# Kernel optimization log

Measured on AMD Instinct MI355X. Metric: run time of the kernel, lower is better.

Reference implementation:

```python
import jax, jax.numpy as jnp
import numpy as np

D_MODEL = 1024
D_FF = 4096
N_HEADS = 16
D_HEAD = D_MODEL // N_HEADS
BSZ, SEQ = 2, 2048
EPS = 1e-6


def layer_norm(x, lam, beta):
    # torch impl: (x - mu) / (std_biased + eps) * lambda + beta
    mu = jnp.mean(x, axis=-1, keepdims=True)
    sigma = jnp.sqrt(jnp.mean((x - mu) ** 2, axis=-1, keepdims=True)) + EPS
    return (x - mu) / sigma * lam + beta


def setup_inputs() -> dict:
    key = jax.random.key(0)
    ks = jax.random.split(key, 10)
    s = 0.02
    x = jax.random.normal(ks[0], (BSZ, SEQ, D_MODEL), dtype=jnp.float32)
    mask = jnp.ones((BSZ, 1, 1, SEQ), dtype=jnp.int32)
    # nn.Linear weights stored [out, in]; y = x @ W.T
    Wq = jax.random.normal(ks[1], (D_MODEL, D_MODEL), dtype=jnp.float32) * s
    Wk = jax.random.normal(ks[2], (D_MODEL, D_MODEL), dtype=jnp.float32) * s
    Wv = jax.random.normal(ks[3], (D_MODEL, D_MODEL), dtype=jnp.float32) * s
    Wo = jax.random.normal(ks[4], (D_MODEL, D_MODEL), dtype=jnp.float32) * s
    w1 = jax.random.normal(ks[5], (D_FF, D_MODEL), dtype=jnp.float32) * s
    b1 = jnp.zeros((D_FF,), dtype=jnp.float32)
    w2 = jax.random.normal(ks[6], (D_MODEL, D_FF), dtype=jnp.float32) * s
    b2 = jnp.zeros((D_MODEL,), dtype=jnp.float32)
    g1 = jnp.ones((D_MODEL,), dtype=jnp.float32)
    be1 = jnp.zeros((D_MODEL,), dtype=jnp.float32)
    g2 = jnp.ones((D_MODEL,), dtype=jnp.float32)
    be2 = jnp.zeros((D_MODEL,), dtype=jnp.float32)
    return {"x": x, "mask": mask, "Wq": Wq, "Wk": Wk, "Wv": Wv, "Wo": Wo,
            "w1": w1, "b1": b1, "w2": w2, "b2": b2,
            "g1": g1, "be1": be1, "g2": g2, "be2": be2}


def reference(x, mask, Wq, Wk, Wv, Wo, w1, b1, w2, b2, g1, be1, g2, be2):
    b, s, _ = x.shape
    # projections (y = x @ W.T), split heads -> [b, h, s, dh]
    def split_heads(t):
        return t.reshape(b, s, N_HEADS, D_HEAD).transpose(0, 2, 1, 3)
    Q = split_heads(x @ Wq.T)
    K = split_heads(x @ Wk.T)
    V = split_heads(x @ Wv.T)
    score = jnp.einsum('bhqd,bhkd->bhqk', Q, K) / jnp.sqrt(jnp.float32(D_HEAD))
    score = jnp.where(mask == 0, -jnp.inf, score)
    attn = jax.nn.softmax(score, axis=-1)
    out = jnp.einsum('bhqk,bhkd->bhqd', attn, V)
    out = out.transpose(0, 2, 1, 3).reshape(b, s, D_MODEL)
    x1 = out @ Wo.T
    x2 = layer_norm(x1 + x, g1, be1)
    x3 = jax.nn.relu(x2 @ w1.T + b1) @ w2.T + b2
    x4 = layer_norm(x2 + x3, g2, be2)
    return x4
```

## Files before the change

### kernel.cpp

```cpp
#include <hip/hip_runtime.h>
#include <math.h>

typedef __attribute__((ext_vector_type(8))) short bf16x8;
typedef __attribute__((ext_vector_type(4))) float f32x4;
typedef __attribute__((ext_vector_type(8))) unsigned short us8;
typedef unsigned short u16;
typedef unsigned int u32;

constexpr int BSZ = 2, SEQ = 2048, DM = 1024, DFF = 4096, NH = 16, DH = 64;
constexpr int MROWS = BSZ * SEQ;

__device__ __forceinline__ float bf2f(u16 u) {
  union { unsigned int i; float f; } v; v.i = ((unsigned int)u) << 16; return v.f;
}
__device__ __forceinline__ u16 f2bf(float f) {
  union { float f; unsigned int i; } v; v.f = f;
  unsigned int r = v.i + 0x7fffu + ((v.i >> 16) & 1u);
  return (u16)(r >> 16);
}

#define GLOAD16(gp, lp) __builtin_amdgcn_global_load_lds( \
    (const __attribute__((address_space(1))) void*)(gp),  \
    (__attribute__((address_space(3))) void*)(lp), 16, 0, 0)
#define GLOAD4(gp, lp) __builtin_amdgcn_global_load_lds( \
    (const __attribute__((address_space(1))) void*)(gp),  \
    (__attribute__((address_space(3))) void*)(lp), 4, 0, 0)

__global__ __launch_bounds__(256) void cvt_bf16(const float* __restrict__ in,
                                                u16* __restrict__ out, int n) {
  const int i = (blockIdx.x * 256 + threadIdx.x) * 8;
  if (i >= n) return;
  const float4 a = *(const float4*)(in + i);
  const float4 b = *(const float4*)(in + i + 4);
  uint4 o;
  o.x = f2bf(a.x) | ((unsigned)f2bf(a.y) << 16);
  o.y = f2bf(a.z) | ((unsigned)f2bf(a.w) << 16);
  o.z = f2bf(b.x) | ((unsigned)f2bf(b.y) << 16);
  o.w = f2bf(b.z) | ((unsigned)f2bf(b.w) << 16);
  *(uint4*)(out + i) = o;
}

template <int BM, int BN, bool BIAS, bool RELU, bool OBF16>
__global__ __launch_bounds__(256) void gemm_bf16(
    const u16* __restrict__ A, const u16* __restrict__ B,
    const float* __restrict__ bias, float* __restrict__ Cf,
    u16* __restrict__ Cb, int M, int N, int K) {
  constexpr int MI = BM / 32, NI = BN / 32;
  __shared__ u16 As[2][BM * 32];
  __shared__ u16 Bs[2][BN * 32];
  const int tid = threadIdx.x;
  const int lane = tid & 63, wid = tid >> 6;

  const int nwg = gridDim.x * gridDim.y;
  int id = blockIdx.y * gridDim.x + blockIdx.x;
  id = (id & 7) * (nwg >> 3) + (id >> 3);
  const int bx = id % gridDim.x, by = id / gridDim.x;

  const int row0 = by * BM, col0 = bx * BN;
  const int wr = (wid >> 1) * (BM / 2), wc = (wid & 1) * (BN / 2);
  const int fr = lane & 15, hi = lane >> 4;

  f32x4 acc[MI][NI];
#pragma unroll
  for (int i = 0; i < MI; ++i)
#pragma unroll
    for (int j = 0; j < NI; ++j) acc[i][j] = {0.f, 0.f, 0.f, 0.f};

  const int sr = tid >> 2;
  const int se = (tid & 3) * 8;

#define STAGE(buf, k0)                                                        \
  {                                                                           \
    _Pragma("unroll")                                                         \
    for (int c = 0; c < BM * 64; c += 4096) {                                 \
      const int r = (c >> 6) + sr;                                            \
      GLOAD16(A + (size_t)(row0 + r) * K + ((k0) + se),                       \
              ((char*)As[buf]) + c + tid * 16);                               \
    }                                                                         \
    _Pragma("unroll")                                                         \
    for (int c = 0; c < BN * 64; c += 4096) {                                 \
      const int r = (c >> 6) + sr;                                            \
      GLOAD16(B + (size_t)(col0 + r) * K + ((k0) + se),                       \
              ((char*)Bs[buf]) + c + tid * 16);                               \
    }                                                                         \
  }

  STAGE(0, 0);
  __syncthreads();

  const int NIT = K / 32;
  for (int it = 0; it < NIT; ++it) {
    const int cur = it & 1;
    if (it + 1 < NIT) STAGE(cur ^ 1, (it + 1) * 32);

    bf16x8 af[MI], bv[NI];
#pragma unroll
    for (int mi = 0; mi < MI; ++mi)
      af[mi] = *(const bf16x8*)&As[cur][(wr + mi * 16 + fr) * 32 + hi * 8];
#pragma unroll
    for (int ni = 0; ni < NI; ++ni)
      bv[ni] = *(const bf16x8*)&Bs[cur][(wc + ni * 16 + fr) * 32 + hi * 8];
#pragma unroll
    for (int mi = 0; mi < MI; ++mi)
#pragma unroll
      for (int ni = 0; ni < NI; ++ni)
        acc[mi][ni] = __builtin_amdgcn_mfma_f32_16x16x32_bf16(
            af[mi], bv[ni], acc[mi][ni], 0, 0, 0);
    __syncthreads();
  }
#undef STAGE

  const int erow = row0 + wr + (hi << 2);
  const int ecol0 = col0 + wc;
#pragma unroll
  for (int ni = 0; ni < NI; ++ni) {
    const int col = ecol0 + ni * 16 + fr;
    const float bvv = BIAS ? bias[col] : 0.f;
#pragma unroll
    for (int mi = 0; mi < MI; ++mi) {
      const int rbase = erow + mi * 16;
#pragma unroll
      for (int j = 0; j < 4; ++j) {
        float v = acc[mi][ni][j] + bvv;
        if (RELU) v = fmaxf(v, 0.f);
        const size_t idx = (size_t)(rbase + j) * N + col;
        if (OBF16) Cb[idx] = f2bf(v); else Cf[idx] = v;
      }
    }
  }
}

__global__ __launch_bounds__(256) void attn_mfma(
    const u16* __restrict__ QKV, const int* __restrict__ mask,
    u16* __restrict__ Ob) {
  constexpr int KB = 64, QB = 64, NT = SEQ / KB;
  __shared__ u16 Kl[2][KB * 64];
  __shared__ u16 Vt[2][64 * KB];
  __shared__ int ml[2][KB];

  const int tid = threadIdx.x;
  const int lane = tid & 63, wid = tid >> 6;
  const int q0 = blockIdx.x * QB;
  const int bh = blockIdx.y;
  const int b = bh >> 4, h = bh & 15;
  const size_t base = (size_t)b * SEQ * 3072;
  const int fr = lane & 15, g = lane >> 4;

  const u16* qp = QKV + base + (size_t)(q0 + wid * 16 + fr) * 3072 + h * 64 + g * 8;
  const bf16x8 qf0 = *(const bf16x8*)qp;
  const bf16x8 qf1 = *(const bf16x8*)(qp + 32);

  const int krow = wid * 16 + (lane >> 3);
  const int kcol = 8 * ((lane & 7) ^ (lane >> 3));
  const u16* ksrc = QKV + base + 1024 + h * 64 + kcol;
  const int kdst = wid * 2048 + lane * 16;

  const int va = tid >> 3;
  const int vq = tid & 7;
  const u16* vsrc = QKV + base + 2048 + h * 64 + vq * 8;

  f32x4 o[4] = {{0.f,0.f,0.f,0.f},{0.f,0.f,0.f,0.f},{0.f,0.f,0.f,0.f},{0.f,0.f,0.f,0.f}};
  float mreg = -3e38f, lreg = 0.f;

  {
    GLOAD16(ksrc + (size_t)krow * 3072, (char*)Kl[0] + kdst);
    GLOAD16(ksrc + (size_t)(krow + 8) * 3072, (char*)Kl[0] + kdst + 1024);
    if (wid == 0) GLOAD4(mask + b * SEQ + lane, (char*)ml[0] + lane * 4);
    const us8 v0 = *(const us8*)(vsrc + (size_t)(2 * va) * 3072);
    const us8 v1 = *(const us8*)(vsrc + (size_t)(2 * va + 1) * 3072);
    char* vb = (char*)Vt[0];
#pragma unroll
    for (int i = 0; i < 8; ++i) {
      const int d = vq * 8 + i;
      const u32 wv = (u32)(u16)v0[i] | ((u32)(u16)v1[i] << 16);
      *(u32*)(vb + d * 128 + ((4 * va) ^ ((vq ^ i) << 4))) = wv;
    }
  }
  __syncthreads();

  for (int it = 0; it < NT; ++it) {
    const int cur = it & 1, nxt = cur ^ 1;
    const int ktn = (it + 1) * KB;
    const bool pre = (it + 1 < NT);
    us8 v0 = {}, v1 = {};
    if (pre) {
      GLOAD16(ksrc + (size_t)(ktn + krow) * 3072, (char*)Kl[nxt] + kdst);
      GLOAD16(ksrc + (size_t)(ktn + krow + 8) * 3072, (char*)Kl[nxt] + kdst + 1024);
      if (wid == 0) GLOAD4(mask + b * SEQ + ktn + lane, (char*)ml[nxt] + lane * 4);
      v0 = *(const us8*)(vsrc + (size_t)(ktn + 2 * va) * 3072);
      v1 = *(const us8*)(vsrc + (size_t)(ktn + 2 * va + 1) * 3072);
    }

    f32x4 s[4];
#pragma unroll
    for (int t16 = 0; t16 < 4; ++t16) {
      const int kr = t16 * 16 + fr;
      const char* krp = (const char*)Kl[cur] + kr * 128;
      const int sw = (kr & 7) << 4;
      const bf16x8 kf0 = *(const bf16x8*)(krp + ((g * 16) ^ sw));
      const bf16x8 kf1 = *(const bf16x8*)(krp + ((g * 16 + 64) ^ sw));
      f32x4 a = {0.f, 0.f, 0.f, 0.f};
      a = __builtin_amdgcn_mfma_f32_16x16x32_bf16(kf0, qf0, a, 0, 0, 0);
      a = __builtin_amdgcn_mfma_f32_16x16x32_bf16(kf1, qf1, a, 0, 0, 0);
      s[t16] = a;
    }

#pragma unroll
    for (int t16 = 0; t16 < 4; ++t16) {
      const int4 mv = *(const int4*)&ml[cur][t16 * 16 + g * 4];
      const int* mp = (const int*)&mv;
#pragma unroll
      for (int j = 0; j < 4; ++j)
        s[t16][j] = (mp[j] == 0) ? -3e38f : s[t16][j] * 0.125f;
    }

    float rmax = s[0][0];
#pragma unroll
    for (int t16 = 0; t16 < 4; ++t16)
#pragma unroll
      for (int j = 0; j < 4; ++j) rmax = fmaxf(rmax, s[t16][j]);
    rmax = fmaxf(rmax, __shfl_xor(rmax, 16));
    rmax = fmaxf(rmax, __shfl_xor(rmax, 32));

    if (!__all(rmax <= mreg + 8.f)) {
      const float mn = fmaxf(mreg, rmax);
      const float sc = __expf(mreg - mn);
      mreg = mn;
      lreg *= sc;
#pragma unroll
      for (int j = 0; j < 4; ++j) {
        const float scj = __shfl(sc, (g << 4) + g * 4 + j);
#pragma unroll
        for (int dt = 0; dt < 4; ++dt) o[dt][j] *= scj;
      }
    }

    float p[4][4];
    float rsum = 0.f;
#pragma unroll
    for (int t16 = 0; t16 < 4; ++t16)
#pragma unroll
      for (int j = 0; j < 4; ++j) {
        p[t16][j] = __expf(s[t16][j] - mreg);
        rsum += p[t16][j];
      }
    rsum += __shfl_xor(rsum, 16);
    rsum += __shfl_xor(rsum, 32);
    lreg += rsum;

    u32 plo[4], phi[4];
#pragma unroll
    for (int t16 = 0; t16 < 4; ++t16) {
      asm("v_cvt_pk_bf16_f32 %0, %1, %2"
          : "=v"(plo[t16]) : "v"(p[t16][0]), "v"(p[t16][1]));
      asm("v_cvt_pk_bf16_f32 %0, %1, %2"
          : "=v"(phi[t16]) : "v"(p[t16][2]), "v"(p[t16][3]));
    }

#pragma unroll
    for (int kh = 0; kh < 2; ++kh) {
      u32 fd[4];
#pragma unroll
      for (int hf = 0; hf < 2; ++hf) {
        const int sl = fr + ((((g & 1) << 1) + hf) << 4);
        const u32 c0l = (u32)__shfl((int)plo[kh * 2], sl);
        const u32 c0h = (u32)__shfl((int)phi[kh * 2], sl);
        const u32 c1l = (u32)__shfl((int)plo[kh * 2 + 1], sl);
        const u32 c1h = (u32)__shfl((int)phi[kh * 2 + 1], sl);
        const bool s1 = ((g >> 1) & 1) != 0;
        fd[hf * 2] = s1 ? c1l : c0l;
        fd[hf * 2 + 1] = s1 ? c1h : c0h;
      }
      union { u32 d[4]; bf16x8 v; } uu;
      uu.d[0] = fd[0]; uu.d[1] = fd[1]; uu.d[2] = fd[2]; uu.d[3] = fd[3];
      const bf16x8 pf = uu.v;
#pragma unroll
      for (int dt = 0; dt < 4; ++dt) {
        const int d = dt * 16 + fr;
        const int xd = (((d >> 3) ^ d) & 7) << 4;
        const bf16x8 vf = *(const bf16x8*)((const char*)Vt[cur] + d * 128 +
                                           ((g * 16 + kh * 64) ^ xd));
        o[dt] = __builtin_amdgcn_mfma_f32_16x16x32_bf16(pf, vf, o[dt], 0, 0, 0);
      }
    }

    if (pre) {
      char* vb = (char*)Vt[nxt];
#pragma unroll
      for (int i = 0; i < 8; ++i) {
        const int d = vq * 8 + i;
        const u32 wv = (u32)(u16)v0[i] | ((u32)(u16)v1[i] << 16);
        *(u32*)(vb + d * 128 + ((4 * va) ^ ((vq ^ i) << 4))) = wv;
      }
    }
    __syncthreads();
  }

  const float inv = 1.f / lreg;
#pragma unroll
  for (int j = 0; j < 4; ++j) {
    const float invj = __shfl(inv, (g << 4) + g * 4 + j);
    const int qrow = q0 + wid * 16 + g * 4 + j;
    u16* orow = Ob + (size_t)(b * SEQ + qrow) * DM + h * 64;
#pragma unroll
    for (int dt = 0; dt < 4; ++dt)
      orow[dt * 16 + fr] = f2bf(o[dt][j] * invj);
  }
}

template <bool ABF, bool OBF>
__global__ __launch_bounds__(256) void ln_add(const void* __restrict__ Ap,
                                              const float* __restrict__ Bx,
                                              const float* __restrict__ g,
                                              const float* __restrict__ be,
                                              void* __restrict__ outp) {
  __shared__ float red[2][4];
  __shared__ float mu_s, sig_s;
  const int row = blockIdx.x;
  const int tid = threadIdx.x;

  float4 a;
  if (ABF) {
    const u16* ap = (const u16*)Ap + (size_t)row * DM + tid * 4;
    const ushort4 u = *(const ushort4*)ap;
    a = make_float4(bf2f(u.x), bf2f(u.y), bf2f(u.z), bf2f(u.w));
  } else {
    a = *(const float4*)((const float*)Ap + (size_t)row * DM + tid * 4);
  }
  const float4 b = *(const float4*)(Bx + (size_t)row * DM + tid * 4);
  float4 s = make_float4(a.x + b.x, a.y + b.y, a.z + b.z, a.w + b.w);

  float sum = s.x + s.y + s.z + s.w;
  float sq = s.x * s.x + s.y * s.y + s.z * s.z + s.w * s.w;
#pragma unroll
  for (int off = 32; off >= 1; off >>= 1) {
    sum += __shfl_xor(sum, off);
    sq += __shfl_xor(sq, off);
  }
  const int wid = tid >> 6;
  if ((tid & 63) == 0) { red[0][wid] = sum; red[1][wid] = sq; }
  __syncthreads();
  if (tid == 0) {
    float ts = red[0][0] + red[0][1] + red[0][2] + red[0][3];
    float tq = red[1][0] + red[1][1] + red[1][2] + red[1][3];
    float mu = ts * (1.f / DM);
    float var = tq * (1.f / DM) - mu * mu;
    mu_s = mu;
    sig_s = sqrtf(fmaxf(var, 0.f)) + 1e-6f;
  }
  __syncthreads();
  const float mu = mu_s, inv = 1.f / sig_s;
  const float4 gv = *(const float4*)(g + tid * 4);
  const float4 bv = *(const float4*)(be + tid * 4);
  float4 o;
  o.x = (s.x - mu) * inv * gv.x + bv.x;
  o.y = (s.y - mu) * inv * gv.y + bv.y;
  o.z = (s.z - mu) * inv * gv.z + bv.z;
  o.w = (s.w - mu) * inv * gv.w + bv.w;
  if (OBF) {
    u16* op = (u16*)outp + (size_t)row * DM + tid * 4;
    ushort4 o4;
    o4.x = f2bf(o.x); o4.y = f2bf(o.y); o4.z = f2bf(o.z); o4.w = f2bf(o.w);
    *(ushort4*)op = o4;
  } else {
    *(float4*)((float*)outp + (size_t)row * DM + tid * 4) = o;
  }
}

extern "C" void kernel_launch(void* const* d_in, const int* in_sizes, int n_in,
                              void* d_out, int out_size, void* d_ws,
                              size_t ws_size, hipStream_t stream) {
  const float* x  = (const float*)d_in[0];
  const int* mask = (const int*)d_in[1];
  const float* Wq = (const float*)d_in[2];
  const float* Wk = (const float*)d_in[3];
  const float* Wv = (const float*)d_in[4];
  const float* Wo = (const float*)d_in[5];
  const float* w1 = (const float*)d_in[6];
  const float* b1 = (const float*)d_in[7];
  const float* w2 = (const float*)d_in[8];
  const float* b2 = (const float*)d_in[9];
  const float* g1 = (const float*)d_in[10];
  const float* be1 = (const float*)d_in[11];
  const float* g2 = (const float*)d_in[12];
  const float* be2 = (const float*)d_in[13];
  float* out = (float*)d_out;
  float* ws = (float*)d_ws;

  u16*   QKVb  = (u16*)(ws + 0);
  u16*   xb    = (u16*)(ws + 6291456);
  u16*   Wqkvb = (u16*)(ws + 8388608);
  u16*   Wob   = (u16*)(ws + 9961472);
  u16*   w1b   = (u16*)(ws + 10485760);
  u16*   w2b   = (u16*)(ws + 12582912);
  u16*   Obf   = (u16*)(ws + 14680064);
  float* X1    = ws + 16777216;
  u16*   X2b   = (u16*)(ws + 20971520);
  float* X3    = ws + 23068672;
  u16*   Hb    = (u16*)(ws + 0);

  const dim3 blk(256);

  cvt_bf16<<<2048, blk, 0, stream>>>(x, xb, MROWS * DM);
  cvt_bf16<<<512,  blk, 0, stream>>>(Wq, Wqkvb, DM * DM);
  cvt_bf16<<<512,  blk, 0, stream>>>(Wk, Wqkvb + DM * DM, DM * DM);
  cvt_bf16<<<512,  blk, 0, stream>>>(Wv, Wqkvb + 2 * DM * DM, DM * DM);
  cvt_bf16<<<512,  blk, 0, stream>>>(Wo, Wob, DM * DM);
  cvt_bf16<<<2048, blk, 0, stream>>>(w1, w1b, DFF * DM);
  cvt_bf16<<<2048, blk, 0, stream>>>(w2, w2b, DM * DFF);

  gemm_bf16<128, 128, false, false, true><<<dim3(3072 / 128, MROWS / 128), blk, 0, stream>>>(
      xb, Wqkvb, nullptr, nullptr, QKVb, MROWS, 3072, DM);

  attn_mfma<<<dim3(SEQ / 64, BSZ * NH), blk, 0, stream>>>(QKVb, mask, Obf);

  gemm_bf16<64, 128, false, false, false><<<dim3(DM / 128, MROWS / 64), blk, 0, stream>>>(
      Obf, Wob, nullptr, X1, nullptr, MROWS, DM, DM);

  ln_add<false, true><<<dim3(MROWS), blk, 0, stream>>>(X1, x, g1, be1, X2b);

  gemm_bf16<128, 128, true, true, true><<<dim3(DFF / 128, MROWS / 128), blk, 0, stream>>>(
      X2b, w1b, b1, nullptr, Hb, MROWS, DFF, DM);

  gemm_bf16<64, 128, true, false, false><<<dim3(DM / 128, MROWS / 64), blk, 0, stream>>>(
      Hb, w2b, b2, X3, nullptr, MROWS, DM, DFF);

  ln_add<true, false><<<dim3(MROWS), blk, 0, stream>>>(X2b, X3, g2, be2, out);
}
```

Measured before the change: 319.0 us.

## Add 256x256-tile 512-thread GEMM kernel for QKV and FFN1 projections

Adds a new bf16 MFMA GEMM kernel that uses 256x256 output tiles, 512 threads (8 waves each computing 128x64), and a split-phase schedule that interleaves the next tile's global-to-LDS loads with MFMA work and raises wave priority around the MFMA bursts. The QKV projection and the first FFN GEMM now use it instead of the 128x128 kernel. The goal is higher arithmetic intensity and fewer global loads per flop. The trade-off is far fewer workgroups (192 and 256 blocks), which may underfill the 256 CUs, plus higher register and LDS pressure.

```diff
diff --git a/kernel.cpp b/kernel.cpp
--- a/kernel.cpp
+++ b/kernel.cpp
@@ -38,6 +38,121 @@
   o.z = f2bf(b.x) | ((unsigned)f2bf(b.y) << 16);
   o.w = f2bf(b.z) | ((unsigned)f2bf(b.w) << 16);
   *(uint4*)(out + i) = o;
+}
+
+template <bool BIAS, bool RELU>
+__global__ __launch_bounds__(512) void gemm256(
+    const u16* __restrict__ A, const u16* __restrict__ B,
+    const float* __restrict__ bias, u16* __restrict__ Cb,
+    int M, int N, int K) {
+  __shared__ u16 As[2][256 * 32];
+  __shared__ u16 Bs[2][256 * 32];
+  const int tid = threadIdx.x;
+  const int lane = tid & 63, wid = tid >> 6;
+
+  const int nwg = gridDim.x * gridDim.y;
+  int id = blockIdx.y * gridDim.x + blockIdx.x;
+  id = (id & 7) * (nwg >> 3) + (id >> 3);
+  const int bx = id % gridDim.x, by = id / gridDim.x;
+
+  const int row0 = by * 256, col0 = bx * 256;
+  const int wrM = (wid >> 2) * 128;
+  const int wc = (wid & 3) * 64;
+  const int fr = lane & 15, hi = lane >> 4;
+
+  f32x4 acc[8][4];
+#pragma unroll
+  for (int i = 0; i < 8; ++i)
+#pragma unroll
+    for (int j = 0; j < 4; ++j) acc[i][j] = {0.f, 0.f, 0.f, 0.f};
+
+  const int srow = tid >> 2;
+  const int sch = tid & 3;
+
+#define STAGE_A(buf, k0)                                                      \
+  {                                                                           \
+    _Pragma("unroll")                                                         \
+    for (int r = 0; r < 2; ++r) {                                             \
+      const int row = r * 128 + srow;                                         \
+      GLOAD16(A + (size_t)(row0 + row) * K + (k0) + sch * 8,                  \
+              ((char*)As[buf]) + row * 64 + sch * 16);                        \
+    }                                                                         \
+  }
+#define STAGE_B(buf, k0)                                                      \
+  {                                                                           \
+    _Pragma("unroll")                                                         \
+    for (int r = 0; r < 2; ++r) {                                             \
+      const int row = r * 128 + srow;                                         \
+      GLOAD16(B + (size_t)(col0 + row) * K + (k0) + sch * 8,                  \
+              ((char*)Bs[buf]) + row * 64 + sch * 16);                        \
+    }                                                                         \
+  }
+
+  STAGE_A(0, 0);
+  STAGE_B(0, 0);
+  __syncthreads();
+
+  const int NT = K / 32;
+  for (int t = 0; t < NT; ++t) {
+    const int cur = t & 1, nxt = cur ^ 1;
+    const bool pre = (t + 1 < NT);
+    const int k0n = (t + 1) * 32;
+
+    if (pre) STAGE_A(nxt, k0n);
+    bf16x8 bfr[4], afr[4];
+#pragma unroll
+    for (int ni = 0; ni < 4; ++ni)
+      bfr[ni] = *(const bf16x8*)&Bs[cur][(wc + ni * 16 + fr) * 32 + hi * 8];
+#pragma unroll
+    for (int m = 0; m < 4; ++m)
+      afr[m] = *(const bf16x8*)&As[cur][(wrM + m * 16 + fr) * 32 + hi * 8];
+    asm volatile("s_waitcnt lgkmcnt(0)" ::: "memory");
+    __builtin_amdgcn_sched_barrier(0);
+    __builtin_amdgcn_s_setprio(1);
+#pragma unroll
+    for (int m = 0; m < 4; ++m)
+#pragma unroll
+      for (int ni = 0; ni < 4; ++ni)
+        acc[m][ni] = __builtin_amdgcn_mfma_f32_16x16x32_bf16(
+            afr[m], bfr[ni], acc[m][ni], 0, 0, 0);
+    __builtin_amdgcn_s_setprio(0);
+    __builtin_amdgcn_s_barrier();
+
+    if (pre) STAGE_B(nxt, k0n);
+#pragma unroll
+    for (int m = 0; m < 4; ++m)
+      afr[m] = *(const bf16x8*)&As[cur][(wrM + 64 + m * 16 + fr) * 32 + hi * 8];
+    asm volatile("s_waitcnt lgkmcnt(0)" ::: "memory");
+    __builtin_amdgcn_sched_barrier(0);
+    __builtin_amdgcn_s_setprio(1);
+#pragma unroll
+    for (int m = 0; m < 4; ++m)
+#pragma unroll
+      for (int ni = 0; ni < 4; ++ni)
+        acc[4 + m][ni] = __builtin_amdgcn_mfma_f32_16x16x32_bf16(
+            afr[m], bfr[ni], acc[4 + m][ni], 0, 0, 0);
+    __builtin_amdgcn_s_setprio(0);
+    asm volatile("s_waitcnt vmcnt(0)" ::: "memory");
+    __builtin_amdgcn_s_barrier();
+  }
+#undef STAGE_A
+#undef STAGE_B
+
+  const int erow0 = row0 + wrM + hi * 4;
+#pragma unroll
+  for (int ni = 0; ni < 4; ++ni) {
+    const int col = col0 + wc + ni * 16 + fr;
+    const float bvv = BIAS ? bias[col] : 0.f;
+#pragma unroll
+    for (int mi = 0; mi < 8; ++mi) {
+#pragma unroll
+      for (int j = 0; j < 4; ++j) {
+        float v = acc[mi][ni][j] + bvv;
+        if (RELU) v = fmaxf(v, 0.f);
+        Cb[(size_t)(erow0 + mi * 16 + j) * N + col] = f2bf(v);
+      }
+    }
+  }
 }
 
 template <int BM, int BN, bool BIAS, bool RELU, bool OBF16>
@@ -400,6 +515,7 @@
   u16*   Hb    = (u16*)(ws + 0);
 
   const dim3 blk(256);
+  const dim3 blk512(512);
 
   cvt_bf16<<<2048, blk, 0, stream>>>(x, xb, MROWS * DM);
   cvt_bf16<<<512,  blk, 0, stream>>>(Wq, Wqkvb, DM * DM);
@@ -409,8 +525,8 @@
   cvt_bf16<<<2048, blk, 0, stream>>>(w1, w1b, DFF * DM);
   cvt_bf16<<<2048, blk, 0, stream>>>(w2, w2b, DM * DFF);
 
-  gemm_bf16<128, 128, false, false, true><<<dim3(3072 / 128, MROWS / 128), blk, 0, stream>>>(
-      xb, Wqkvb, nullptr, nullptr, QKVb, MROWS, 3072, DM);
+  gemm256<false, false><<<dim3(3072 / 256, MROWS / 256), blk512, 0, stream>>>(
+      xb, Wqkvb, nullptr, QKVb, MROWS, 3072, DM);
 
   attn_mfma<<<dim3(SEQ / 64, BSZ * NH), blk, 0, stream>>>(QKVb, mask, Obf);
 
@@ -419,8 +535,8 @@
 
   ln_add<false, true><<<dim3(MROWS), blk, 0, stream>>>(X1, x, g1, be1, X2b);
 
-  gemm_bf16<128, 128, true, true, true><<<dim3(DFF / 128, MROWS / 128), blk, 0, stream>>>(
-      X2b, w1b, b1, nullptr, Hb, MROWS, DFF, DM);
+  gemm256<true, true><<<dim3(DFF / 256, MROWS / 256), blk512, 0, stream>>>(
+      X2b, w1b, b1, Hb, MROWS, DFF, DM);
 
   gemm_bf16<64, 128, true, false, false><<<dim3(DM / 128, MROWS / 64), blk, 0, stream>>>(
       Hb, w2b, b2, X3, nullptr, MROWS, DM, DFF);
```

Result: slower. 337.4 us (+5.8%).
